# Performance work log

Measured on AMD Instinct MI355X. Metric: run time of the kernel, lower is better.

## Reference

```python
import jax, jax.numpy as jnp
import numpy as np

HIDDEN = 1024
SENT = 1024
NS = 8192
NK = 8192


def setup_inputs() -> dict:
    key = jax.random.key(0)
    ks = jax.random.split(key, 6)
    scale = 0.02
    return {
        "sentences_embedding": jax.random.normal(ks[0], (NS, SENT), dtype=jnp.float32),
        "knowledge_embedding": jax.random.normal(ks[1], (NK, 2 * HIDDEN), dtype=jnp.float32),
        "Ws": jax.random.normal(ks[2], (HIDDEN, SENT), dtype=jnp.float32) * scale,
        "bs": jnp.zeros((HIDDEN,), dtype=jnp.float32),
        "Wk": jax.random.normal(ks[3], (HIDDEN, 2 * HIDDEN), dtype=jnp.float32) * scale,
        "bk": jnp.zeros((HIDDEN,), dtype=jnp.float32),
    }


def reference(sentences_embedding, knowledge_embedding, Ws, bs, Wk, bk):
    # S: [Ns, hidden], K: [Nk, hidden] (torch Linear: x @ W.T + b)
    S = sentences_embedding @ Ws.T + bs
    K = knowledge_embedding @ Wk.T + bk
    V = knowledge_embedding  # [Nk, 2*hidden]
    scores = S @ K.T  # [Ns, Nk]
    # NOTE: softmax over dim=0 (across sentences), per the original module
    attns = jax.nn.softmax(scores, axis=0)
    fused_knowledge = attns @ V  # [Ns, 2*hidden]
    return (attns, fused_knowledge)
```

## Files before the change

kernel.cpp:

```cpp
#include <hip/hip_runtime.h>
#include <hip/hip_bf16.h>
#include <math.h>

typedef __bf16 bf16_t;
typedef __bf16 bf16x8 __attribute__((ext_vector_type(8)));
typedef __bf16 bf16x4v __attribute__((ext_vector_type(4)));
typedef float floatx4 __attribute__((ext_vector_type(4)));

#define BM 128
#define BN 128
#define BK 64
#define LDT 72

__device__ __forceinline__ void gload_lds16(const void* g, void* l) {
    __builtin_amdgcn_global_load_lds(
        (__attribute__((address_space(1))) void*)g,
        (__attribute__((address_space(3))) void*)l,
        16, 0, 0);
}

__device__ __forceinline__ void split8(const float* p, bf16x8& hi, bf16x8& lo) {
    const float4* q = (const float4*)p;
    float4 a = q[0], b = q[1];
    float v[8] = { a.x, a.y, a.z, a.w, b.x, b.y, b.z, b.w };
#pragma unroll
    for (int i = 0; i < 8; ++i) {
        bf16_t h = (bf16_t)v[i];
        hi[i] = h;
        lo[i] = (bf16_t)(v[i] - (float)h);
    }
}

template<bool OUT_SPLIT, bool HAS_BIAS>
__global__ __launch_bounds__(256, 2)
void gemm_nt_split(const float* __restrict__ A, const float* __restrict__ B,
                   const float* __restrict__ bias,
                   void* __restrict__ C0, bf16_t* __restrict__ Clo,
                   int M, int N, int K)
{
    __shared__ bf16_t Ah[BM * LDT];
    __shared__ bf16_t Al[BM * LDT];
    __shared__ bf16_t Bh[BN * LDT];
    __shared__ bf16_t Bl[BN * LDT];

    const int t    = threadIdx.x;
    const int m0   = blockIdx.x * BM;
    const int n0   = blockIdx.y * BN;
    const int lane = t & 63;
    const int wm   = ((t >> 6) & 1) * 64;
    const int wn   = (t >> 7) * 64;
    const int lr   = lane & 15;
    const int lg   = lane >> 4;

    floatx4 acc[4][4] = {};

    for (int k0 = 0; k0 < K; k0 += BK) {
#pragma unroll
        for (int i = 0; i < 4; ++i) {
            int idx = t + i * 256;
            int row = idx >> 3;
            int col = (idx & 7) << 3;
            bf16x8 h, l;
            split8(&A[(size_t)(m0 + row) * K + k0 + col], h, l);
            *(bf16x8*)&Ah[row * LDT + col] = h;
            *(bf16x8*)&Al[row * LDT + col] = l;
            split8(&B[(size_t)(n0 + row) * K + k0 + col], h, l);
            *(bf16x8*)&Bh[row * LDT + col] = h;
            *(bf16x8*)&Bl[row * LDT + col] = l;
        }
        __syncthreads();
#pragma unroll
        for (int ks = 0; ks < BK; ks += 32) {
            bf16x8 ah[4], al[4], bh[4], bl[4];
#pragma unroll
            for (int mi = 0; mi < 4; ++mi) {
                ah[mi] = *(const bf16x8*)&Ah[(wm + mi * 16 + lr) * LDT + ks + lg * 8];
                al[mi] = *(const bf16x8*)&Al[(wm + mi * 16 + lr) * LDT + ks + lg * 8];
            }
#pragma unroll
            for (int ni = 0; ni < 4; ++ni) {
                bh[ni] = *(const bf16x8*)&Bh[(wn + ni * 16 + lr) * LDT + ks + lg * 8];
                bl[ni] = *(const bf16x8*)&Bl[(wn + ni * 16 + lr) * LDT + ks + lg * 8];
            }
#pragma unroll
            for (int mi = 0; mi < 4; ++mi)
#pragma unroll
                for (int ni = 0; ni < 4; ++ni) {
                    acc[mi][ni] = __builtin_amdgcn_mfma_f32_16x16x32_bf16(ah[mi], bh[ni], acc[mi][ni], 0, 0, 0);
                    acc[mi][ni] = __builtin_amdgcn_mfma_f32_16x16x32_bf16(ah[mi], bl[ni], acc[mi][ni], 0, 0, 0);
                    acc[mi][ni] = __builtin_amdgcn_mfma_f32_16x16x32_bf16(al[mi], bh[ni], acc[mi][ni], 0, 0, 0);
                }
        }
        __syncthreads();
    }

#pragma unroll
    for (int mi = 0; mi < 4; ++mi)
#pragma unroll
        for (int ni = 0; ni < 4; ++ni) {
            int col = n0 + wn + ni * 16 + lr;
            float bv = 0.0f;
            if constexpr (HAS_BIAS) bv = bias[col];
#pragma unroll
            for (int r = 0; r < 4; ++r) {
                int row = m0 + wm + mi * 16 + lg * 4 + r;
                float v = acc[mi][ni][r] + bv;
                if constexpr (OUT_SPLIT) {
                    bf16_t h = (bf16_t)v;
                    ((bf16_t*)C0)[(size_t)row * N + col] = h;
                    Clo[(size_t)row * N + col] = (bf16_t)(v - (float)h);
                } else {
                    ((float*)C0)[(size_t)row * N + col] = v;
                }
            }
        }
}

__global__ __launch_bounds__(256, 2)
void gemm_nt_pre_async(const bf16_t* __restrict__ Ahi, const bf16_t* __restrict__ Alo,
                       const bf16_t* __restrict__ Bhi, const bf16_t* __restrict__ Blo,
                       float* __restrict__ C, float* __restrict__ pm,
                       float* __restrict__ pz, int M, int N, int K)
{
    __shared__ bf16_t Ah[BM * BK];
    __shared__ bf16_t Al[BM * BK];
    __shared__ bf16_t Bh[BN * BK];
    __shared__ bf16_t Bl[BN * BK];
    __shared__ float red_m[2][128];
    __shared__ float red_z[2][128];

    const int t    = threadIdx.x;
    const int m0   = blockIdx.x * BM;
    const int n0   = blockIdx.y * BN;
    const int lane = t & 63;
    const int wv   = t >> 6;
    const int widm = (t >> 6) & 1;
    const int wm   = widm * 64;
    const int wn   = (t >> 7) * 64;
    const int lr   = lane & 15;
    const int lg   = lane >> 4;
    const int lrow = lane >> 3;
    const int lcol = (((lane & 7) ^ lrow) * 8);
    const int swz  = (lr & 7) << 3;

    floatx4 acc[4][4] = {};

    for (int k0 = 0; k0 < K; k0 += BK) {
#pragma unroll
        for (int i = 0; i < 4; ++i) {
            const int seg = wv * 4 + i;
            const int row = seg * 8 + lrow;
            const size_t ga = (size_t)(m0 + row) * K + k0 + lcol;
            const size_t gb = (size_t)(n0 + row) * K + k0 + lcol;
            gload_lds16(&Ahi[ga], &Ah[seg * 512]);
            gload_lds16(&Alo[ga], &Al[seg * 512]);
            gload_lds16(&Bhi[gb], &Bh[seg * 512]);
            gload_lds16(&Blo[gb], &Bl[seg * 512]);
        }
        __syncthreads();
#pragma unroll
        for (int ks = 0; ks < BK; ks += 32) {
            const int cA = (ks + lg * 8) ^ swz;
            bf16x8 ah[4], al[4], bh[4], bl[4];
#pragma unroll
            for (int mi = 0; mi < 4; ++mi) {
                ah[mi] = *(const bf16x8*)&Ah[(wm + mi * 16 + lr) * BK + cA];
                al[mi] = *(const bf16x8*)&Al[(wm + mi * 16 + lr) * BK + cA];
            }
#pragma unroll
            for (int ni = 0; ni < 4; ++ni) {
                bh[ni] = *(const bf16x8*)&Bh[(wn + ni * 16 + lr) * BK + cA];
                bl[ni] = *(const bf16x8*)&Bl[(wn + ni * 16 + lr) * BK + cA];
            }
#pragma unroll
            for (int mi = 0; mi < 4; ++mi)
#pragma unroll
                for (int ni = 0; ni < 4; ++ni) {
                    acc[mi][ni] = __builtin_amdgcn_mfma_f32_16x16x32_bf16(ah[mi], bh[ni], acc[mi][ni], 0, 0, 0);
                    acc[mi][ni] = __builtin_amdgcn_mfma_f32_16x16x32_bf16(ah[mi], bl[ni], acc[mi][ni], 0, 0, 0);
                    acc[mi][ni] = __builtin_amdgcn_mfma_f32_16x16x32_bf16(al[mi], bh[ni], acc[mi][ni], 0, 0, 0);
                }
        }
        __syncthreads();
    }

#pragma unroll
    for (int mi = 0; mi < 4; ++mi)
#pragma unroll
        for (int ni = 0; ni < 4; ++ni) {
            int col = n0 + wn + ni * 16 + lr;
#pragma unroll
            for (int r = 0; r < 4; ++r) {
                int row = m0 + wm + mi * 16 + lg * 4 + r;
                C[(size_t)row * N + col] = acc[mi][ni][r];
            }
        }

#pragma unroll
    for (int ni = 0; ni < 4; ++ni) {
        float lm = -INFINITY;
#pragma unroll
        for (int mi = 0; mi < 4; ++mi)
#pragma unroll
            for (int r = 0; r < 4; ++r) lm = fmaxf(lm, acc[mi][ni][r]);
        float lz = 0.0f;
#pragma unroll
        for (int mi = 0; mi < 4; ++mi)
#pragma unroll
            for (int r = 0; r < 4; ++r) lz += __expf(acc[mi][ni][r] - lm);
#pragma unroll
        for (int off = 16; off <= 32; off <<= 1) {
            float om = __shfl_xor(lm, off);
            float oz = __shfl_xor(lz, off);
            float nm = fmaxf(lm, om);
            lz = lz * __expf(lm - nm) + oz * __expf(om - nm);
            lm = nm;
        }
        if (lg == 0) {
            red_m[widm][wn + ni * 16 + lr] = lm;
            red_z[widm][wn + ni * 16 + lr] = lz;
        }
    }
    __syncthreads();
    if (t < 128) {
        float a = red_m[0][t], b = red_m[1][t];
        float za = red_z[0][t], zb = red_z[1][t];
        float mb = fmaxf(a, b);
        float z  = za * __expf(a - mb) + zb * __expf(b - mb);
        pm[(size_t)blockIdx.x * 8192 + n0 + t] = mb;
        pz[(size_t)blockIdx.x * 8192 + n0 + t] = z;
    }
}

__global__ __launch_bounds__(256, 4)
void gemm_nt_bf16_async(const bf16_t* __restrict__ A, const bf16_t* __restrict__ B,
                        float* __restrict__ C, int M, int N, int K)
{
    __shared__ bf16_t As[BM * BK];
    __shared__ bf16_t Bs[BN * BK];

    const int t    = threadIdx.x;
    const int m0   = blockIdx.x * BM;
    const int n0   = blockIdx.y * BN;
    const int lane = t & 63;
    const int wv   = t >> 6;
    const int wm   = ((t >> 6) & 1) * 64;
    const int wn   = (t >> 7) * 64;
    const int lr   = lane & 15;
    const int lg   = lane >> 4;
    const int lrow = lane >> 3;
    const int lcol = (((lane & 7) ^ lrow) * 8);
    const int swz  = (lr & 7) << 3;

    const bf16_t* aBase = A + (size_t)(m0 + wv * 32 + lrow) * K + lcol;
    const bf16_t* bBase = B + (size_t)(n0 + wv * 32 + lrow) * K + lcol;

    floatx4 acc[4][4] = {};

    for (int k0 = 0; k0 < K; k0 += BK) {
#pragma unroll
        for (int i = 0; i < 4; ++i) {
            const int seg = wv * 4 + i;
            gload_lds16(aBase + (size_t)i * 8 * K + k0, &As[seg * 512]);
            gload_lds16(bBase + (size_t)i * 8 * K + k0, &Bs[seg * 512]);
        }
        __syncthreads();
#pragma unroll
        for (int ks = 0; ks < BK; ks += 32) {
            const int cA = (ks + lg * 8) ^ swz;
            bf16x8 a0 = *(const bf16x8*)&As[(wm + 0 * 16 + lr) * BK + cA];
            bf16x8 a1 = *(const bf16x8*)&As[(wm + 1 * 16 + lr) * BK + cA];
            bf16x8 a2 = *(const bf16x8*)&As[(wm + 2 * 16 + lr) * BK + cA];
            bf16x8 a3 = *(const bf16x8*)&As[(wm + 3 * 16 + lr) * BK + cA];
#pragma unroll
            for (int ni = 0; ni < 4; ++ni) {
                bf16x8 b = *(const bf16x8*)&Bs[(wn + ni * 16 + lr) * BK + cA];
                acc[0][ni] = __builtin_amdgcn_mfma_f32_16x16x32_bf16(a0, b, acc[0][ni], 0, 0, 0);
                acc[1][ni] = __builtin_amdgcn_mfma_f32_16x16x32_bf16(a1, b, acc[1][ni], 0, 0, 0);
                acc[2][ni] = __builtin_amdgcn_mfma_f32_16x16x32_bf16(a2, b, acc[2][ni], 0, 0, 0);
                acc[3][ni] = __builtin_amdgcn_mfma_f32_16x16x32_bf16(a3, b, acc[3][ni], 0, 0, 0);
            }
        }
        __syncthreads();
    }

#pragma unroll
    for (int mi = 0; mi < 4; ++mi)
#pragma unroll
        for (int ni = 0; ni < 4; ++ni) {
            int col = n0 + wn + ni * 16 + lr;
#pragma unroll
            for (int r = 0; r < 4; ++r) {
                int row = m0 + wm + mi * 16 + lg * 4 + r;
                C[(size_t)row * N + col] = acc[mi][ni][r];
            }
        }
}

__global__ __launch_bounds__(256)
void transpose_to_bf16(const float* __restrict__ src, bf16_t* __restrict__ dst,
                       int R, int Ccols)
{
    __shared__ float tile[64][65];
    const int r0 = blockIdx.x * 64;
    const int c0 = blockIdx.y * 64;
    const int tr = threadIdx.x >> 4;
    const int tc = (threadIdx.x & 15) * 4;
#pragma unroll
    for (int i = 0; i < 4; ++i) {
        int r = tr + i * 16;
        float4 v = *(const float4*)&src[(size_t)(r0 + r) * Ccols + c0 + tc];
        tile[r][tc + 0] = v.x; tile[r][tc + 1] = v.y;
        tile[r][tc + 2] = v.z; tile[r][tc + 3] = v.w;
    }
    __syncthreads();
#pragma unroll
    for (int i = 0; i < 4; ++i) {
        int c = tr + i * 16;
        bf16x4v o = { (bf16_t)tile[tc + 0][c], (bf16_t)tile[tc + 1][c],
                      (bf16_t)tile[tc + 2][c], (bf16_t)tile[tc + 3][c] };
        *(bf16x4v*)&dst[(size_t)(c0 + c) * R + r0 + tc] = o;
    }
}

__global__ __launch_bounds__(256)
void col_softmax_combine64(const float* __restrict__ pm, const float* __restrict__ pz,
                           float* __restrict__ mf, float* __restrict__ iz)
{
    int j = blockIdx.x * 256 + threadIdx.x;
    float m = -INFINITY;
#pragma unroll
    for (int c = 0; c < 64; ++c) m = fmaxf(m, pm[(size_t)c * 8192 + j]);
    float z = 0.0f;
#pragma unroll
    for (int c = 0; c < 64; ++c) z += pz[(size_t)c * 8192 + j] * __expf(pm[(size_t)c * 8192 + j] - m);
    mf[j] = m;
    iz[j] = 1.0f / z;
}

__global__ __launch_bounds__(256)
void normalize_attn_bf16(float* __restrict__ sc, const float* __restrict__ mf,
                         const float* __restrict__ iz, bf16_t* __restrict__ ab)
{
    size_t base = ((size_t)blockIdx.x * 256 + threadIdx.x) * 4;
    int j = (int)(base & 8191);
    float4 s  = *(float4*)&sc[base];
    float4 m4 = *(const float4*)&mf[j];
    float4 z4 = *(const float4*)&iz[j];
    s.x = __expf(s.x - m4.x) * z4.x;
    s.y = __expf(s.y - m4.y) * z4.y;
    s.z = __expf(s.z - m4.z) * z4.z;
    s.w = __expf(s.w - m4.w) * z4.w;
    *(float4*)&sc[base] = s;
    bf16x4v b = { (bf16_t)s.x, (bf16_t)s.y, (bf16_t)s.z, (bf16_t)s.w };
    *(bf16x4v*)&ab[base] = b;
}

extern "C" void kernel_launch(void* const* d_in, const int* in_sizes, int n_in,
                              void* d_out, int out_size, void* d_ws, size_t ws_size,
                              hipStream_t stream) {
    const float* sent  = (const float*)d_in[0];
    const float* knowl = (const float*)d_in[1];
    const float* Ws    = (const float*)d_in[2];
    const float* bs    = (const float*)d_in[3];
    const float* Wk    = (const float*)d_in[4];
    const float* bk    = (const float*)d_in[5];

    float* attns = (float*)d_out;
    float* fused = (float*)d_out + (size_t)8192 * 8192;

    const size_t MB = 1024 * 1024;
    char* ws = (char*)d_ws;
    dim3 blk(256);

    bf16_t* Shi = (bf16_t*)(ws + 0 * MB);
    bf16_t* Slo = (bf16_t*)(ws + 16 * MB);
    bf16_t* Khi = (bf16_t*)(ws + 32 * MB);
    bf16_t* Klo = (bf16_t*)(ws + 48 * MB);
    bf16_t* Ab  = (bf16_t*)(ws);
    bf16_t* Vt  = (bf16_t*)(ws + 128 * MB);
    float*  pm  = (float*)(ws + 160 * MB);
    float*  pz  = (float*)(ws + 162 * MB);
    float*  mf  = (float*)(ws + 164 * MB);
    float*  iz  = mf + 8192;

    gemm_nt_split<true, true><<<dim3(64, 8), blk, 0, stream>>>(
        sent, Ws, bs, Shi, Slo, 8192, 1024, 1024);
    gemm_nt_split<true, true><<<dim3(64, 8), blk, 0, stream>>>(
        knowl, Wk, bk, Khi, Klo, 8192, 1024, 2048);
    gemm_nt_pre_async<<<dim3(64, 64), blk, 0, stream>>>(
        Shi, Slo, Khi, Klo, attns, pm, pz, 8192, 8192, 1024);
    transpose_to_bf16<<<dim3(128, 32), blk, 0, stream>>>(knowl, Vt, 8192, 2048);
    col_softmax_combine64<<<dim3(32), blk, 0, stream>>>(pm, pz, mf, iz);
    normalize_attn_bf16<<<dim3(65536), blk, 0, stream>>>(attns, mf, iz, Ab);
    gemm_nt_bf16_async<<<dim3(64, 16), blk, 0, stream>>>(
        Ab, Vt, fused, 8192, 2048, 8192);
}
```

Measured before the change: 1.265 ms.

## Pre-split projection inputs to bf16 hi/lo and load them with async LDS copies

Splitting the fp32 projection inputs into bf16 hi/lo pairs now happens once, in a separate elementwise kernel, instead of inside each GEMM tile load. The two projection GEMMs read these pre-split buffers through direct global-to-LDS loads, using an XOR-swizzled layout in place of the padded one. This removes the repeated fp32 load-and-convert work per tile, which was re-done for every output tile column. In exchange it adds four extra passes that write about 100MB of temporary data, staged in the attns output buffer before the later kernels overwrite it.

```diff
diff --git a/kernel.cpp b/kernel.cpp
--- a/kernel.cpp
+++ b/kernel.cpp
@@ -10,7 +10,6 @@
 #define BM 128
 #define BN 128
 #define BK 64
-#define LDT 72
 
 __device__ __forceinline__ void gload_lds16(const void* g, void* l) {
     __builtin_amdgcn_global_load_lds(
@@ -31,56 +30,70 @@
     }
 }
 
-template<bool OUT_SPLIT, bool HAS_BIAS>
+__global__ __launch_bounds__(256)
+void split_pair(const float* __restrict__ x, bf16_t* __restrict__ hi,
+                bf16_t* __restrict__ lo)
+{
+    size_t i = ((size_t)blockIdx.x * 256 + threadIdx.x) * 8;
+    bf16x8 h, l;
+    split8(&x[i], h, l);
+    *(bf16x8*)&hi[i] = h;
+    *(bf16x8*)&lo[i] = l;
+}
+
 __global__ __launch_bounds__(256, 2)
-void gemm_nt_split(const float* __restrict__ A, const float* __restrict__ B,
-                   const float* __restrict__ bias,
-                   void* __restrict__ C0, bf16_t* __restrict__ Clo,
-                   int M, int N, int K)
-{
-    __shared__ bf16_t Ah[BM * LDT];
-    __shared__ bf16_t Al[BM * LDT];
-    __shared__ bf16_t Bh[BN * LDT];
-    __shared__ bf16_t Bl[BN * LDT];
+void gemm_nt_pre_split_out(const bf16_t* __restrict__ Ahi, const bf16_t* __restrict__ Alo,
+                           const bf16_t* __restrict__ Bhi, const bf16_t* __restrict__ Blo,
+                           const float* __restrict__ bias,
+                           bf16_t* __restrict__ Chi, bf16_t* __restrict__ Clo,
+                           int M, int N, int K)
+{
+    __shared__ bf16_t Ah[BM * BK];
+    __shared__ bf16_t Al[BM * BK];
+    __shared__ bf16_t Bh[BN * BK];
+    __shared__ bf16_t Bl[BN * BK];
 
     const int t    = threadIdx.x;
     const int m0   = blockIdx.x * BM;
     const int n0   = blockIdx.y * BN;
     const int lane = t & 63;
+    const int wv   = t >> 6;
     const int wm   = ((t >> 6) & 1) * 64;
     const int wn   = (t >> 7) * 64;
     const int lr   = lane & 15;
     const int lg   = lane >> 4;
+    const int lrow = lane >> 3;
+    const int lcol = (((lane & 7) ^ lrow) * 8);
+    const int swz  = (lr & 7) << 3;
 
     floatx4 acc[4][4] = {};
 
     for (int k0 = 0; k0 < K; k0 += BK) {
 #pragma unroll
         for (int i = 0; i < 4; ++i) {
-            int idx = t + i * 256;
-            int row = idx >> 3;
-            int col = (idx & 7) << 3;
-            bf16x8 h, l;
-            split8(&A[(size_t)(m0 + row) * K + k0 + col], h, l);
-            *(bf16x8*)&Ah[row * LDT + col] = h;
-            *(bf16x8*)&Al[row * LDT + col] = l;
-            split8(&B[(size_t)(n0 + row) * K + k0 + col], h, l);
-            *(bf16x8*)&Bh[row * LDT + col] = h;
-            *(bf16x8*)&Bl[row * LDT + col] = l;
+            const int seg = wv * 4 + i;
+            const int row = seg * 8 + lrow;
+            const size_t ga = (size_t)(m0 + row) * K + k0 + lcol;
+            const size_t gb = (size_t)(n0 + row) * K + k0 + lcol;
+            gload_lds16(&Ahi[ga], &Ah[seg * 512]);
+            gload_lds16(&Alo[ga], &Al[seg * 512]);
+            gload_lds16(&Bhi[gb], &Bh[seg * 512]);
+            gload_lds16(&Blo[gb], &Bl[seg * 512]);
         }
         __syncthreads();
 #pragma unroll
         for (int ks = 0; ks < BK; ks += 32) {
+            const int cA = (ks + lg * 8) ^ swz;
             bf16x8 ah[4], al[4], bh[4], bl[4];
 #pragma unroll
             for (int mi = 0; mi < 4; ++mi) {
-                ah[mi] = *(const bf16x8*)&Ah[(wm + mi * 16 + lr) * LDT + ks + lg * 8];
-                al[mi] = *(const bf16x8*)&Al[(wm + mi * 16 + lr) * LDT + ks + lg * 8];
+                ah[mi] = *(const bf16x8*)&Ah[(wm + mi * 16 + lr) * BK + cA];
+                al[mi] = *(const bf16x8*)&Al[(wm + mi * 16 + lr) * BK + cA];
             }
 #pragma unroll
             for (int ni = 0; ni < 4; ++ni) {
-                bh[ni] = *(const bf16x8*)&Bh[(wn + ni * 16 + lr) * LDT + ks + lg * 8];
-                bl[ni] = *(const bf16x8*)&Bl[(wn + ni * 16 + lr) * LDT + ks + lg * 8];
+                bh[ni] = *(const bf16x8*)&Bh[(wn + ni * 16 + lr) * BK + cA];
+                bl[ni] = *(const bf16x8*)&Bl[(wn + ni * 16 + lr) * BK + cA];
             }
 #pragma unroll
             for (int mi = 0; mi < 4; ++mi)
@@ -99,19 +112,14 @@
 #pragma unroll
         for (int ni = 0; ni < 4; ++ni) {
             int col = n0 + wn + ni * 16 + lr;
-            float bv = 0.0f;
-            if constexpr (HAS_BIAS) bv = bias[col];
+            float bv = bias[col];
 #pragma unroll
             for (int r = 0; r < 4; ++r) {
                 int row = m0 + wm + mi * 16 + lg * 4 + r;
                 float v = acc[mi][ni][r] + bv;
-                if constexpr (OUT_SPLIT) {
-                    bf16_t h = (bf16_t)v;
-                    ((bf16_t*)C0)[(size_t)row * N + col] = h;
-                    Clo[(size_t)row * N + col] = (bf16_t)(v - (float)h);
-                } else {
-                    ((float*)C0)[(size_t)row * N + col] = v;
-                }
+                bf16_t h = (bf16_t)v;
+                Chi[(size_t)row * N + col] = h;
+                Clo[(size_t)row * N + col] = (bf16_t)(v - (float)h);
             }
         }
 }
@@ -384,10 +392,24 @@
     float*  mf  = (float*)(ws + 164 * MB);
     float*  iz  = mf + 8192;
 
-    gemm_nt_split<true, true><<<dim3(64, 8), blk, 0, stream>>>(
-        sent, Ws, bs, Shi, Slo, 8192, 1024, 1024);
-    gemm_nt_split<true, true><<<dim3(64, 8), blk, 0, stream>>>(
-        knowl, Wk, bk, Khi, Klo, 8192, 1024, 2048);
+    char* sc = (char*)attns;
+    bf16_t* SEhi = (bf16_t*)(sc + 0 * MB);
+    bf16_t* SElo = (bf16_t*)(sc + 16 * MB);
+    bf16_t* KNhi = (bf16_t*)(sc + 32 * MB);
+    bf16_t* KNlo = (bf16_t*)(sc + 64 * MB);
+    bf16_t* Wshi = (bf16_t*)(sc + 96 * MB);
+    bf16_t* Wslo = (bf16_t*)(sc + 98 * MB);
+    bf16_t* Wkhi = (bf16_t*)(sc + 100 * MB);
+    bf16_t* Wklo = (bf16_t*)(sc + 104 * MB);
+
+    split_pair<<<dim3(4096), blk, 0, stream>>>(sent,  SEhi, SElo);
+    split_pair<<<dim3(8192), blk, 0, stream>>>(knowl, KNhi, KNlo);
+    split_pair<<<dim3(512),  blk, 0, stream>>>(Ws,    Wshi, Wslo);
+    split_pair<<<dim3(1024), blk, 0, stream>>>(Wk,    Wkhi, Wklo);
+    gemm_nt_pre_split_out<<<dim3(64, 8), blk, 0, stream>>>(
+        SEhi, SElo, Wshi, Wslo, bs, Shi, Slo, 8192, 1024, 1024);
+    gemm_nt_pre_split_out<<<dim3(64, 8), blk, 0, stream>>>(
+        KNhi, KNlo, Wkhi, Wklo, bk, Khi, Klo, 8192, 1024, 2048);
     gemm_nt_pre_async<<<dim3(64, 64), blk, 0, stream>>>(
         Shi, Slo, Khi, Klo, attns, pm, pz, 8192, 8192, 1024);
     transpose_to_bf16<<<dim3(128, 32), blk, 0, stream>>>(knowl, Vt, 8192, 2048);
```

Result: no change. 1.274 ms (+0.7%).
